# Optimization experiments

Hardware: AMD Instinct MI355X
Metric: run time of the kernel (lower is better)

The kernel has to match this reference:

```python
import jax, jax.numpy as jnp
import numpy as np

NUM_SELECTOR_BITS = 25  # num_of_weights = 26 -> tree depth 25, input width 2**25 - 1


def _mux(s, a, b):
    # Mux(s, a, b) = 0.5 * (s*a - s*b + a + b) = ((1+s)*a + (1-s)*b) / 2
    return 0.5 * (s * a - s * b + a + b)


def setup_inputs() -> dict:
    key = jax.random.key(0)
    k1, k2, k3 = jax.random.split(key, 3)
    n = NUM_SELECTOR_BITS
    x = jax.random.normal(k1, (2 ** n - 1,), dtype=jnp.float32)
    # parameters, init per torch.nn.init.normal_(mean=0, std=0.02)
    trained_const_weight = 0.02 * jax.random.normal(k2, (1,), dtype=jnp.float32)
    mux_selector_weights = 0.02 * jax.random.normal(k3, (n,), dtype=jnp.float32)
    return {
        "x": x,
        "trained_const_weight": trained_const_weight,
        "mux_selector_weights": mux_selector_weights,
    }


def reference(x, trained_const_weight, mux_selector_weights):
    n = mux_selector_weights.shape[0]
    full = 2 ** n - 1
    pad = full - x.shape[0]
    if pad > 0:
        prev = jnp.concatenate([x, jnp.full((pad,), -1.0, dtype=x.dtype)])
    else:
        prev = x
    # Layer 0: padded input has odd length 2**n - 1; the last mux pairs the
    # final element with the trained constant weight (original code's special case).
    a = prev[0::2]                                   # [2**(n-1)]
    b = jnp.concatenate([prev[1::2], trained_const_weight])  # [2**(n-1)]
    prev = _mux(mux_selector_weights[0], a, b)
    # Remaining layers: even-length butterfly reduction, one shared selector per layer.
    for sel in range(1, n):
        prev = _mux(mux_selector_weights[sel], prev[0::2], prev[1::2])
    return prev[0]
```

## Files before the change

kernel.cpp:

```cpp
#include <hip/hip_runtime.h>


__global__ __launch_bounds__(256) void k1(const float* __restrict__ x,
                                          const float* __restrict__ cw,
                                          const float* __restrict__ w,
                                          float* __restrict__ part) {
    float cA[13], cB[13];
#pragma unroll
    for (int l = 0; l < 13; ++l) {
        float s = w[l];
        cA[l] = 0.5f * (1.0f + s);
        cB[l] = 0.5f * (1.0f - s);
    }
    const int t = threadIdx.x;
    const long long gt = (long long)blockIdx.x * 256 + t;
    const long long base = gt * 32;
    const long long LASTGT = (1LL << 25) / 32 - 1;

    float v[32];
    if (gt != LASTGT) {
#pragma unroll
        for (int j = 0; j < 8; ++j) {
            float4 f = *reinterpret_cast<const float4*>(x + base + j * 4);
            v[4 * j + 0] = f.x; v[4 * j + 1] = f.y;
            v[4 * j + 2] = f.z; v[4 * j + 3] = f.w;
        }
    } else {
#pragma unroll
        for (int j = 0; j < 7; ++j) {
            float4 f = *reinterpret_cast<const float4*>(x + base + j * 4);
            v[4 * j + 0] = f.x; v[4 * j + 1] = f.y;
            v[4 * j + 2] = f.z; v[4 * j + 3] = f.w;
        }
        v[28] = x[base + 28];
        v[29] = x[base + 29];
        v[30] = x[base + 30];
        v[31] = cw[0];
    }

#pragma unroll
    for (int l = 0, n = 32; n > 1; n >>= 1, ++l) {
#pragma unroll
        for (int i = 0; i < n / 2; ++i)
            v[i] = cA[l] * v[2 * i] + cB[l] * v[2 * i + 1];
    }
    float val = v[0];

#pragma unroll
    for (int k = 0; k < 6; ++k) {
        const int l = 5 + k;
        float other = __shfl_xor(val, 1 << k, 64);
        bool upper = (t >> k) & 1;
        float a = upper ? other : val;
        float b = upper ? val : other;
        val = cA[l] * a + cB[l] * b;
    }

    __shared__ float lds[4];
    if ((t & 63) == 0) lds[t >> 6] = val;
    __syncthreads();
    if (t == 0) {
        float p01 = cA[11] * lds[0] + cB[11] * lds[1];
        float p23 = cA[11] * lds[2] + cB[11] * lds[3];
        part[blockIdx.x] = cA[12] * p01 + cB[12] * p23;
    }
}

__global__ __launch_bounds__(256) void k2(const float* __restrict__ part,
                                          const float* __restrict__ w,
                                          float* __restrict__ out) {
    float cA[12], cB[12];
#pragma unroll
    for (int l = 0; l < 12; ++l) {
        float s = w[13 + l];
        cA[l] = 0.5f * (1.0f + s);
        cB[l] = 0.5f * (1.0f - s);
    }
    const int t = threadIdx.x;
    float v[16];
#pragma unroll
    for (int j = 0; j < 4; ++j) {
        float4 f = *reinterpret_cast<const float4*>(part + t * 16 + j * 4);
        v[4 * j + 0] = f.x; v[4 * j + 1] = f.y;
        v[4 * j + 2] = f.z; v[4 * j + 3] = f.w;
    }
#pragma unroll
    for (int l = 0, n = 16; n > 1; n >>= 1, ++l) {
#pragma unroll
        for (int i = 0; i < n / 2; ++i)
            v[i] = cA[l] * v[2 * i] + cB[l] * v[2 * i + 1];
    }
    float val = v[0];
#pragma unroll
    for (int k = 0; k < 6; ++k) {
        const int l = 4 + k;
        float other = __shfl_xor(val, 1 << k, 64);
        bool upper = (t >> k) & 1;
        float a = upper ? other : val;
        float b = upper ? val : other;
        val = cA[l] * a + cB[l] * b;
    }
    __shared__ float lds[4];
    if ((t & 63) == 0) lds[t >> 6] = val;
    __syncthreads();
    if (t == 0) {
        float p01 = cA[10] * lds[0] + cB[10] * lds[1];
        float p23 = cA[10] * lds[2] + cB[10] * lds[3];
        out[0] = cA[11] * p01 + cB[11] * p23;
    }
}

extern "C" void kernel_launch(void* const* d_in, const int* in_sizes, int n_in,
                              void* d_out, int out_size, void* d_ws, size_t ws_size,
                              hipStream_t stream) {
    const float* x  = (const float*)d_in[0];
    const float* cw = (const float*)d_in[1];
    const float* w  = (const float*)d_in[2];
    float* part = (float*)d_ws;

    k1<<<4096, 256, 0, stream>>>(x, cw, w, part);
    k2<<<1, 256, 0, stream>>>(part, w, (float*)d_out);
}
```

Baseline: 190.2 us.

## Use coalesced strided float4 loads and fold upper tree levels into weighted accumulation

Each thread now reads eight float4 chunks strided by 1024 elements, so a wavefront's loads are contiguous, instead of 32 contiguous floats per thread. Because the mux tree is linear, the per-chunk results are combined with precomputed products of the level 10-12 coefficients and accumulated with FMA, which renumbers the tree levels in the shuffle and LDS stages. This removes uncoalesced per-thread strided access and register pressure from the 32-element array. It relies on reassociating the linear tree, which changes floating-point rounding order slightly.

```diff
diff --git a/kernel.cpp b/kernel.cpp
--- a/kernel.cpp
+++ b/kernel.cpp
@@ -1,5 +1,4 @@
 #include <hip/hip_runtime.h>
-
 
 __global__ __launch_bounds__(256) void k1(const float* __restrict__ x,
                                           const float* __restrict__ cw,
@@ -12,57 +11,57 @@
         cA[l] = 0.5f * (1.0f + s);
         cB[l] = 0.5f * (1.0f - s);
     }
+    float ic[8];
+#pragma unroll
+    for (int i = 0; i < 8; ++i) {
+        float c = ((i & 1) ? cB[10] : cA[10]);
+        c *= ((i & 2) ? cB[11] : cA[11]);
+        c *= ((i & 4) ? cB[12] : cA[12]);
+        ic[i] = c;
+    }
     const int t = threadIdx.x;
-    const long long gt = (long long)blockIdx.x * 256 + t;
-    const long long base = gt * 32;
-    const long long LASTGT = (1LL << 25) / 32 - 1;
+    const int b = blockIdx.x;
+    const int blockBase = b * 8192;
+    float acc = 0.0f;
 
-    float v[32];
-    if (gt != LASTGT) {
 #pragma unroll
-        for (int j = 0; j < 8; ++j) {
-            float4 f = *reinterpret_cast<const float4*>(x + base + j * 4);
-            v[4 * j + 0] = f.x; v[4 * j + 1] = f.y;
-            v[4 * j + 2] = f.z; v[4 * j + 3] = f.w;
+    for (int it = 0; it < 8; ++it) {
+        const int e = blockBase + it * 1024 + t * 4;
+        float fx, fy, fz, fw;
+        if (it == 7 && b == 4095) {
+            if (t == 255) {
+                fx = x[e]; fy = x[e + 1]; fz = x[e + 2]; fw = cw[0];
+            } else {
+                float4 f = *reinterpret_cast<const float4*>(x + e);
+                fx = f.x; fy = f.y; fz = f.z; fw = f.w;
+            }
+        } else {
+            float4 f = *reinterpret_cast<const float4*>(x + e);
+            fx = f.x; fy = f.y; fz = f.z; fw = f.w;
         }
-    } else {
-#pragma unroll
-        for (int j = 0; j < 7; ++j) {
-            float4 f = *reinterpret_cast<const float4*>(x + base + j * 4);
-            v[4 * j + 0] = f.x; v[4 * j + 1] = f.y;
-            v[4 * j + 2] = f.z; v[4 * j + 3] = f.w;
-        }
-        v[28] = x[base + 28];
-        v[29] = x[base + 29];
-        v[30] = x[base + 30];
-        v[31] = cw[0];
+        float p = cA[1] * (cA[0] * fx + cB[0] * fy) +
+                  cB[1] * (cA[0] * fz + cB[0] * fw);
+        acc = fmaf(ic[it], p, acc);
     }
 
-#pragma unroll
-    for (int l = 0, n = 32; n > 1; n >>= 1, ++l) {
-#pragma unroll
-        for (int i = 0; i < n / 2; ++i)
-            v[i] = cA[l] * v[2 * i] + cB[l] * v[2 * i + 1];
-    }
-    float val = v[0];
-
+    float val = acc;
 #pragma unroll
     for (int k = 0; k < 6; ++k) {
-        const int l = 5 + k;
+        const int l = 2 + k;
         float other = __shfl_xor(val, 1 << k, 64);
         bool upper = (t >> k) & 1;
         float a = upper ? other : val;
-        float b = upper ? val : other;
-        val = cA[l] * a + cB[l] * b;
+        float bb = upper ? val : other;
+        val = cA[l] * a + cB[l] * bb;
     }
 
     __shared__ float lds[4];
     if ((t & 63) == 0) lds[t >> 6] = val;
     __syncthreads();
     if (t == 0) {
-        float p01 = cA[11] * lds[0] + cB[11] * lds[1];
-        float p23 = cA[11] * lds[2] + cB[11] * lds[3];
-        part[blockIdx.x] = cA[12] * p01 + cB[12] * p23;
+        float p01 = cA[8] * lds[0] + cB[8] * lds[1];
+        float p23 = cA[8] * lds[2] + cB[8] * lds[3];
+        part[b] = cA[9] * p01 + cB[9] * p23;
     }
 }
 
@@ -97,8 +96,8 @@
         float other = __shfl_xor(val, 1 << k, 64);
         bool upper = (t >> k) & 1;
         float a = upper ? other : val;
-        float b = upper ? val : other;
-        val = cA[l] * a + cB[l] * b;
+        float bb = upper ? val : other;
+        val = cA[l] * a + cB[l] * bb;
     }
     __shared__ float lds[4];
     if ((t & 63) == 0) lds[t >> 6] = val;
```

Result: no change. 189.9 us (-0.2%).
